# Performance work log

Hardware: AMD Instinct MI355X
Metric: run time of the kernel (lower is better)

## Reference

```python
import jax, jax.numpy as jnp
import numpy as np

N = 1024
D_X = 128
D_Y = 128
NUM_STEPS = 200


def setup_inputs() -> dict:
    key = jax.random.key(0)
    k1, k2, k3, k4, k5 = jax.random.split(key, 5)
    init_samples_x = jax.random.normal(k1, (N, D_X), dtype=jnp.float32)
    init_samples_y = jax.random.normal(k2, (N, D_Y), dtype=jnp.float32)
    mean_final = jax.random.normal(k3, (D_X,), dtype=jnp.float32)
    # variance must be positive and bounded away from zero
    var_final = jax.random.uniform(k4, (D_X,), dtype=jnp.float32, minval=0.25, maxval=0.75)
    gammas = jnp.linspace(1e-3, 1e-2, NUM_STEPS, dtype=jnp.float32)
    # pre-generated per-step Gaussian noise (replaces torch.randn inside the loop)
    noise = jax.random.normal(k5, (NUM_STEPS, N, D_X), dtype=jnp.float32)
    return {
        "init_samples_x": init_samples_x,
        "init_samples_y": init_samples_y,
        "mean_final": mean_final,
        "var_final": var_final,
        "gammas": gammas,
        "noise": noise,
    }


def reference(init_samples_x, init_samples_y, mean_final, var_final, gammas, noise):
    """Faithful JAX port of Langevin.record_init_langevin.

    grad_gauss(x, m, v) = -(x - m) / v
    per step k:
        t_old = x + gamma_k * grad_gauss(x)
        x     = t_old + sqrt(2*gamma_k) * z_k
        t_new = x + gamma_k * grad_gauss(x)
        record x, y, t_old - t_new
    """
    num_steps = gammas.shape[0]
    n = init_samples_x.shape[0]

    def step(x, inp):
        gamma, z = inp
        t_old = x + gamma * (-(x - mean_final) / var_final)
        x_new = t_old + jnp.sqrt(2.0 * gamma) * z
        t_new = x_new + gamma * (-(x_new - mean_final) / var_final)
        return x_new, (x_new, t_old - t_new)

    _, (xs, outs) = jax.lax.scan(step, init_samples_x, (gammas, noise))
    # scan stacks along leading (step) axis -> [S, N, D]; match torch layout [N, S, D]
    x_tot = jnp.transpose(xs, (1, 0, 2))
    out = jnp.transpose(outs, (1, 0, 2))
    # y is constant across steps; the torch loop just replicates it
    y_tot = jnp.broadcast_to(init_samples_y[:, None, :], (n, num_steps, init_samples_y.shape[1]))
    steps_expanded = jnp.broadcast_to(
        jnp.arange(num_steps, dtype=jnp.int32)[None, :, None], (n, num_steps, 1)
    )
    return x_tot, y_tot, out, steps_expanded
```

## Files before the change

### kernel.cpp

```cpp
#include <hip/hip_runtime.h>
#include <math.h>

constexpr int N   = 1024;
constexpr int D   = 128;
constexpr int S   = 200;
constexpr int D2  = D / 2;
constexpr int ND2 = N * D2;
constexpr int CHAIN_BLOCKS = (N * D2) / 256;
constexpr int SEG = 8;
constexpr int L   = S / SEG;
constexpr int PF1 = 10;
constexpr int PF2 = 5;
constexpr int PF  = 8;

typedef float f2 __attribute__((ext_vector_type(2)));
typedef float f4 __attribute__((ext_vector_type(4)));

__global__ __launch_bounds__(256, 4) void boundary_kernel(
    const f2* __restrict__ x0,
    const f2* __restrict__ mean,
    const f2* __restrict__ var,
    const float* __restrict__ gammas,
    const f2* __restrict__ noise,
    f2* __restrict__ bnd)
{
    __shared__ float sg[S];
    __shared__ float ss[S];
    for (int i = threadIdx.x; i < S; i += 256) {
        float g = gammas[i];
        sg[i] = g;
        ss[i] = sqrtf(2.0f * g);
    }
    __syncthreads();

    const int idx = blockIdx.x * 256 + threadIdx.x;
    const int dp  = idx & 63;

    f2 x        = x0[idx];
    const f2 m  = mean[dp];
    const f2 v  = var[dp];
    const float ivx = 1.0f / v.x;
    const float ivy = 1.0f / v.y;

    const f2* zp = noise + idx;

    f2 zb[PF1];
    #pragma unroll
    for (int i = 0; i < PF1; ++i) zb[i] = zp[(size_t)i * ND2];

    #pragma unroll 1
    for (int kb = 0; kb < S; kb += PF1) {
        f2 zn[PF1];
        if (kb + PF1 < S) {
            #pragma unroll
            for (int i = 0; i < PF1; ++i)
                zn[i] = zp[(size_t)(kb + PF1 + i) * ND2];
        }
        #pragma unroll
        for (int i = 0; i < PF1; ++i) {
            const int k = kb + i;
            const float g = sg[k];
            const float s = ss[k];
            const float gx = g * ivx;
            const float gy = g * ivy;
            x.x = fmaf(s, zb[i].x, fmaf(-gx, x.x - m.x, x.x));
            x.y = fmaf(s, zb[i].y, fmaf(-gy, x.y - m.y, x.y));
            if (((k + 1) % L) == 0 && (k + 1) < S)
                bnd[(size_t)((k + 1) / L - 1) * ND2 + idx] = x;
        }
        #pragma unroll
        for (int i = 0; i < PF1; ++i) zb[i] = zn[i];
    }
}

__global__ __launch_bounds__(256, 6) void segment_kernel(
    const f2* __restrict__ x0,
    const f4* __restrict__ y0,
    const f2* __restrict__ mean,
    const f2* __restrict__ var,
    const float* __restrict__ gammas,
    const f2* __restrict__ noise,
    const f2* __restrict__ bnd,
    f2* __restrict__ x_tot,
    f4* __restrict__ y_tot,
    f2* __restrict__ outp,
    float* __restrict__ steps)
{
    if (blockIdx.x >= SEG * CHAIN_BLOCKS) {
        const int n   = blockIdx.x - SEG * CHAIN_BLOCKS;
        const int t   = threadIdx.x;
        const int col = t & 31;
        const int r0  = t >> 5;
        const f4  yv  = y0[(size_t)n * 32 + col];
        f4* yq = y_tot + (size_t)n * (S * 32);
        #pragma unroll
        for (int j = 0; j < S / 8; ++j) {
            const int k = r0 + j * 8;
            __builtin_nontemporal_store(yv, &yq[(size_t)k * 32 + col]);
        }
        if (t < S) steps[(size_t)n * S + t] = (float)t;
        return;
    }

    __shared__ float sg[L];
    __shared__ float ss[L];
    const int seg = blockIdx.x / CHAIN_BLOCKS;
    const int rb  = blockIdx.x % CHAIN_BLOCKS;
    const int k0  = seg * L;
    if (threadIdx.x < L) {
        float g = gammas[k0 + threadIdx.x];
        sg[threadIdx.x] = g;
        ss[threadIdx.x] = sqrtf(2.0f * g);
    }
    __syncthreads();

    const int idx = rb * 256 + threadIdx.x;
    const int n   = idx >> 6;
    const int dp  = idx & 63;

    f2 x = (seg == 0) ? x0[idx] : bnd[(size_t)(seg - 1) * ND2 + idx];
    const f2 m  = mean[dp];
    const f2 v  = var[dp];
    const float ivx = 1.0f / v.x;
    const float ivy = 1.0f / v.y;

    const f2* zp = noise + (size_t)k0 * ND2 + idx;
    f2* xq = x_tot + (size_t)n * (S * D2) + (size_t)k0 * D2 + dp;
    f2* oq = outp  + (size_t)n * (S * D2) + (size_t)k0 * D2 + dp;

    f2 zb[PF2];
    #pragma unroll
    for (int i = 0; i < PF2; ++i) zb[i] = zp[(size_t)i * ND2];

    #pragma unroll 1
    for (int kb = 0; kb < L; kb += PF2) {
        f2 zn[PF2];
        if (kb + PF2 < L) {
            #pragma unroll
            for (int i = 0; i < PF2; ++i)
                zn[i] = zp[(size_t)(kb + PF2 + i) * ND2];
        }
        #pragma unroll
        for (int i = 0; i < PF2; ++i) {
            const int k = kb + i;
            const float g = sg[k];
            const float s = ss[k];
            const float gx = g * ivx;
            const float gy = g * ivy;

            const float tox = fmaf(-gx, x.x - m.x, x.x);
            const float toy = fmaf(-gy, x.y - m.y, x.y);
            x.x = fmaf(s, zb[i].x, tox);
            x.y = fmaf(s, zb[i].y, toy);
            const float tnx = fmaf(-gx, x.x - m.x, x.x);
            const float tny = fmaf(-gy, x.y - m.y, x.y);

            f2 o;
            o.x = tox - tnx;
            o.y = toy - tny;

            __builtin_nontemporal_store(x, &xq[(size_t)k * D2]);
            __builtin_nontemporal_store(o, &oq[(size_t)k * D2]);
        }
        #pragma unroll
        for (int i = 0; i < PF2; ++i) zb[i] = zn[i];
    }
}

__global__ __launch_bounds__(256, 4) void langevin_kernel(
    const f2* __restrict__ x0,
    const f4* __restrict__ y0,
    const f2* __restrict__ mean,
    const f2* __restrict__ var,
    const float* __restrict__ gammas,
    const f2* __restrict__ noise,
    f2* __restrict__ x_tot,
    f4* __restrict__ y_tot,
    f2* __restrict__ outp,
    float* __restrict__ steps)
{
    if (blockIdx.x >= CHAIN_BLOCKS) {
        const int n   = blockIdx.x - CHAIN_BLOCKS;
        const int t   = threadIdx.x;
        const int col = t & 31;
        const int r0  = t >> 5;
        const f4  yv  = y0[(size_t)n * 32 + col];
        f4* yq = y_tot + (size_t)n * (S * 32);
        #pragma unroll
        for (int j = 0; j < S / 8; ++j) {
            const int k = r0 + j * 8;
            __builtin_nontemporal_store(yv, &yq[(size_t)k * 32 + col]);
        }
        if (t < S) steps[(size_t)n * S + t] = (float)t;
        return;
    }

    __shared__ float sg[S];
    __shared__ float ss[S];
    for (int i = threadIdx.x; i < S; i += 256) {
        float g = gammas[i];
        sg[i] = g;
        ss[i] = sqrtf(2.0f * g);
    }
    __syncthreads();

    const int idx = blockIdx.x * 256 + threadIdx.x;
    const int n   = idx >> 6;
    const int dp  = idx & 63;

    f2 x        = x0[idx];
    const f2 m  = mean[dp];
    const f2 v  = var[dp];
    const float ivx = 1.0f / v.x;
    const float ivy = 1.0f / v.y;

    const f2* zp = noise + idx;
    f2* xq = x_tot + (size_t)n * (S * D2) + dp;
    f2* oq = outp  + (size_t)n * (S * D2) + dp;

    f2 zb[PF];
    #pragma unroll
    for (int i = 0; i < PF; ++i)
        zb[i] = __builtin_nontemporal_load(&zp[(size_t)i * ND2]);

    #pragma unroll 1
    for (int kb = 0; kb < S; kb += PF) {
        f2 zn[PF];
        if (kb + PF < S) {
            #pragma unroll
            for (int i = 0; i < PF; ++i)
                zn[i] = __builtin_nontemporal_load(&zp[(size_t)(kb + PF + i) * ND2]);
        }
        #pragma unroll
        for (int i = 0; i < PF; ++i) {
            const int k = kb + i;
            const float g = sg[k];
            const float s = ss[k];
            const float gx = g * ivx;
            const float gy = g * ivy;

            const float tox = fmaf(-gx, x.x - m.x, x.x);
            const float toy = fmaf(-gy, x.y - m.y, x.y);
            x.x = fmaf(s, zb[i].x, tox);
            x.y = fmaf(s, zb[i].y, toy);
            const float tnx = fmaf(-gx, x.x - m.x, x.x);
            const float tny = fmaf(-gy, x.y - m.y, x.y);

            f2 o;
            o.x = tox - tnx;
            o.y = toy - tny;

            __builtin_nontemporal_store(x, &xq[(size_t)k * D2]);
            __builtin_nontemporal_store(o, &oq[(size_t)k * D2]);
        }
        #pragma unroll
        for (int i = 0; i < PF; ++i) zb[i] = zn[i];
    }
}

extern "C" void kernel_launch(void* const* d_in, const int* in_sizes, int n_in,
                              void* d_out, int out_size, void* d_ws, size_t ws_size,
                              hipStream_t stream)
{
    const float* x0     = (const float*)d_in[0];
    const float* y0     = (const float*)d_in[1];
    const float* mean   = (const float*)d_in[2];
    const float* var    = (const float*)d_in[3];
    const float* gammas = (const float*)d_in[4];
    const float* noise  = (const float*)d_in[5];

    float* x_tot = (float*)d_out;
    float* y_tot = x_tot + (size_t)N * S * D;
    float* outp  = y_tot + (size_t)N * S * D;
    float* steps = outp  + (size_t)N * S * D;

    const size_t need = (size_t)(SEG - 1) * ND2 * sizeof(f2);
    if (d_ws != nullptr && ws_size >= need) {
        boundary_kernel<<<CHAIN_BLOCKS, 256, 0, stream>>>(
            (const f2*)x0, (const f2*)mean, (const f2*)var, gammas,
            (const f2*)noise, (f2*)d_ws);
        segment_kernel<<<SEG * CHAIN_BLOCKS + N, 256, 0, stream>>>(
            (const f2*)x0, (const f4*)y0, (const f2*)mean, (const f2*)var,
            gammas, (const f2*)noise, (const f2*)d_ws,
            (f2*)x_tot, (f4*)y_tot, (f2*)outp, steps);
    } else {
        langevin_kernel<<<CHAIN_BLOCKS + N, 256, 0, stream>>>(
            (const f2*)x0, (const f4*)y0, (const f2*)mean, (const f2*)var,
            gammas, (const f2*)noise,
            (f2*)x_tot, (f4*)y_tot, (f2*)outp, steps);
    }
}
```

Measured before the change: 399.6 us.

## Replace sequential boundary pass with parallel linear-recurrence prefix via partial sums

The serial boundary kernel, which walked all 200 steps per element to get segment start values, is replaced by a closed-form solution of the affine recurrence. A tiny single-block kernel precomputes cumulative products and offsets in double precision. A segment-parallel kernel computes weighted noise partial sums per segment, and the emit kernel combines the earlier partials to get each segment's starting x. This removes the long serial dependency chain but adds an extra full read of the noise, double-precision arithmetic, and possible numerical drift from the 1/P scaling.

Result: slower. 460.6 us (+15.3%).

```diff
diff --git a/kernel.cpp b/kernel.cpp
--- a/kernel.cpp
+++ b/kernel.cpp
@@ -9,78 +9,101 @@
 constexpr int CHAIN_BLOCKS = (N * D2) / 256;
 constexpr int SEG = 8;
 constexpr int L   = S / SEG;
-constexpr int PF1 = 10;
 constexpr int PF2 = 5;
 constexpr int PF  = 8;
 
-typedef float f2 __attribute__((ext_vector_type(2)));
-typedef float f4 __attribute__((ext_vector_type(4)));
-
-__global__ __launch_bounds__(256, 4) void boundary_kernel(
-    const f2* __restrict__ x0,
+typedef float  f2 __attribute__((ext_vector_type(2)));
+typedef float  f4 __attribute__((ext_vector_type(4)));
+typedef double d2 __attribute__((ext_vector_type(2)));
+
+constexpr size_t PT_OFF   = 0;
+constexpr size_t QT_OFF   = (size_t)S * D2;
+constexpr size_t CT_OFF   = (size_t)2 * S * D2;
+constexpr size_t PART_OFF = (size_t)3 * S * D2;
+constexpr size_t WS_D2    = PART_OFF + (size_t)SEG * ND2;
+
+__global__ __launch_bounds__(64, 1) void precompute_kernel(
+    const f2* __restrict__ var,
     const f2* __restrict__ mean,
-    const f2* __restrict__ var,
     const float* __restrict__ gammas,
+    d2* __restrict__ ws)
+{
+    const int dp = threadIdx.x;
+    d2* PT = ws + PT_OFF;
+    d2* QT = ws + QT_OFF;
+    d2* CT = ws + CT_OFF;
+
+    const f2 vv = var[dp];
+    const f2 mm = mean[dp];
+    const double vx = vv.x, vy = vv.y, mx = mm.x, my = mm.y;
+    double Px = 1.0, Py = 1.0, Qx = 0.0, Qy = 0.0;
+
+    for (int j = 0; j < S; ++j) {
+        const double g  = (double)gammas[j];
+        Px *= (1.0 - g / vx);
+        Py *= (1.0 - g / vy);
+        const double rx = 1.0 / Px, ry = 1.0 / Py;
+        const double s  = sqrt(2.0 * g);
+        d2 ct; ct.x = s * rx;           ct.y = s * ry;           CT[(size_t)j * D2 + dp] = ct;
+        Qx += (g / vx) * mx * rx;
+        Qy += (g / vy) * my * ry;
+        d2 pt; pt.x = Px; pt.y = Py;    PT[(size_t)j * D2 + dp] = pt;
+        d2 qt; qt.x = Qx; qt.y = Qy;    QT[(size_t)j * D2 + dp] = qt;
+    }
+}
+
+__global__ __launch_bounds__(256, 4) void partial_kernel(
     const f2* __restrict__ noise,
-    f2* __restrict__ bnd)
-{
-    __shared__ float sg[S];
-    __shared__ float ss[S];
-    for (int i = threadIdx.x; i < S; i += 256) {
-        float g = gammas[i];
-        sg[i] = g;
-        ss[i] = sqrtf(2.0f * g);
-    }
-    __syncthreads();
-
-    const int idx = blockIdx.x * 256 + threadIdx.x;
+    d2* __restrict__ ws)
+{
+    const int seg = blockIdx.x / CHAIN_BLOCKS;
+    const int rb  = blockIdx.x % CHAIN_BLOCKS;
+    const int k0  = seg * L;
+    const int idx = rb * 256 + threadIdx.x;
     const int dp  = idx & 63;
 
-    f2 x        = x0[idx];
-    const f2 m  = mean[dp];
-    const f2 v  = var[dp];
-    const float ivx = 1.0f / v.x;
-    const float ivy = 1.0f / v.y;
-
-    const f2* zp = noise + idx;
-
-    f2 zb[PF1];
+    const d2* CT = ws + CT_OFF;
+    const f2* zp = noise + (size_t)k0 * ND2 + idx;
+    const d2* ct = CT + (size_t)k0 * D2 + dp;
+
+    d2 sig; sig.x = 0.0; sig.y = 0.0;
+
+    f2 zb[PF2]; d2 cb[PF2];
     #pragma unroll
-    for (int i = 0; i < PF1; ++i) zb[i] = zp[(size_t)i * ND2];
+    for (int i = 0; i < PF2; ++i) {
+        zb[i] = zp[(size_t)i * ND2];
+        cb[i] = ct[(size_t)i * D2];
+    }
 
     #pragma unroll 1
-    for (int kb = 0; kb < S; kb += PF1) {
-        f2 zn[PF1];
-        if (kb + PF1 < S) {
-            #pragma unroll
-            for (int i = 0; i < PF1; ++i)
-                zn[i] = zp[(size_t)(kb + PF1 + i) * ND2];
-        }
-        #pragma unroll
-        for (int i = 0; i < PF1; ++i) {
-            const int k = kb + i;
-            const float g = sg[k];
-            const float s = ss[k];
-            const float gx = g * ivx;
-            const float gy = g * ivy;
-            x.x = fmaf(s, zb[i].x, fmaf(-gx, x.x - m.x, x.x));
-            x.y = fmaf(s, zb[i].y, fmaf(-gy, x.y - m.y, x.y));
-            if (((k + 1) % L) == 0 && (k + 1) < S)
-                bnd[(size_t)((k + 1) / L - 1) * ND2 + idx] = x;
-        }
-        #pragma unroll
-        for (int i = 0; i < PF1; ++i) zb[i] = zn[i];
-    }
-}
-
-__global__ __launch_bounds__(256, 6) void segment_kernel(
+    for (int kb = 0; kb < L; kb += PF2) {
+        f2 zn[PF2]; d2 cn[PF2];
+        const bool more = (kb + PF2) < L;
+        #pragma unroll
+        for (int i = 0; i < PF2; ++i) {
+            zn[i] = more ? zp[(size_t)(kb + PF2 + i) * ND2] : zb[i];
+            cn[i] = more ? ct[(size_t)(kb + PF2 + i) * D2]  : cb[i];
+        }
+        #pragma unroll
+        for (int i = 0; i < PF2; ++i) {
+            sig.x = fma(cb[i].x, (double)zb[i].x, sig.x);
+            sig.y = fma(cb[i].y, (double)zb[i].y, sig.y);
+        }
+        #pragma unroll
+        for (int i = 0; i < PF2; ++i) { zb[i] = zn[i]; cb[i] = cn[i]; }
+    }
+
+    ws[PART_OFF + (size_t)seg * ND2 + idx] = sig;
+}
+
+__global__ __launch_bounds__(256, 4) void emit_kernel(
     const f2* __restrict__ x0,
     const f4* __restrict__ y0,
     const f2* __restrict__ mean,
     const f2* __restrict__ var,
     const float* __restrict__ gammas,
     const f2* __restrict__ noise,
-    const f2* __restrict__ bnd,
+    const d2* __restrict__ ws,
     f2* __restrict__ x_tot,
     f4* __restrict__ y_tot,
     f2* __restrict__ outp,
@@ -118,33 +141,48 @@
     const int n   = idx >> 6;
     const int dp  = idx & 63;
 
-    f2 x = (seg == 0) ? x0[idx] : bnd[(size_t)(seg - 1) * ND2 + idx];
     const f2 m  = mean[dp];
     const f2 v  = var[dp];
     const float ivx = 1.0f / v.x;
     const float ivy = 1.0f / v.y;
 
-    const f2* zp = noise + (size_t)k0 * ND2 + idx;
+    f2 x;
+    if (seg == 0) {
+        x = x0[idx];
+    } else {
+        d2 W; W.x = 0.0; W.y = 0.0;
+        #pragma unroll 1
+        for (int s2 = 0; s2 < seg; ++s2) {
+            const d2 p = ws[PART_OFF + (size_t)s2 * ND2 + idx];
+            W.x += p.x; W.y += p.y;
+        }
+        const d2 P = ws[PT_OFF + (size_t)(k0 - 1) * D2 + dp];
+        const d2 Q = ws[QT_OFF + (size_t)(k0 - 1) * D2 + dp];
+        const f2 xi = x0[idx];
+        x.x = (float)(P.x * ((double)xi.x + Q.x + W.x));
+        x.y = (float)(P.y * ((double)xi.y + Q.y + W.y));
+    }
+
+    const f2* zq = noise + (size_t)k0 * ND2 + idx;
     f2* xq = x_tot + (size_t)n * (S * D2) + (size_t)k0 * D2 + dp;
     f2* oq = outp  + (size_t)n * (S * D2) + (size_t)k0 * D2 + dp;
 
     f2 zb[PF2];
     #pragma unroll
-    for (int i = 0; i < PF2; ++i) zb[i] = zp[(size_t)i * ND2];
+    for (int i = 0; i < PF2; ++i) zb[i] = zq[(size_t)i * ND2];
 
     #pragma unroll 1
     for (int kb = 0; kb < L; kb += PF2) {
         f2 zn[PF2];
-        if (kb + PF2 < L) {
-            #pragma unroll
-            for (int i = 0; i < PF2; ++i)
-                zn[i] = zp[(size_t)(kb + PF2 + i) * ND2];
-        }
+        const bool more = (k0 + kb + PF2) < S;
+        #pragma unroll
+        for (int i = 0; i < PF2; ++i)
+            zn[i] = more ? zq[(size_t)(kb + PF2 + i) * ND2] : zb[i];
         #pragma unroll
         for (int i = 0; i < PF2; ++i) {
-            const int k = kb + i;
-            const float g = sg[k];
-            const float s = ss[k];
+            const int kk = kb + i;
+            const float g = sg[kk];
+            const float s = ss[kk];
             const float gx = g * ivx;
             const float gy = g * ivy;
 
@@ -159,8 +197,8 @@
             o.x = tox - tnx;
             o.y = toy - tny;
 
-            __builtin_nontemporal_store(x, &xq[(size_t)k * D2]);
-            __builtin_nontemporal_store(o, &oq[(size_t)k * D2]);
+            __builtin_nontemporal_store(x, &xq[(size_t)kk * D2]);
+            __builtin_nontemporal_store(o, &oq[(size_t)kk * D2]);
         }
         #pragma unroll
         for (int i = 0; i < PF2; ++i) zb[i] = zn[i];
@@ -274,14 +312,16 @@
     float* outp  = y_tot + (size_t)N * S * D;
     float* steps = outp  + (size_t)N * S * D;
 
-    const size_t need = (size_t)(SEG - 1) * ND2 * sizeof(f2);
+    const size_t need = WS_D2 * sizeof(d2);
     if (d_ws != nullptr && ws_size >= need) {
-        boundary_kernel<<<CHAIN_BLOCKS, 256, 0, stream>>>(
-            (const f2*)x0, (const f2*)mean, (const f2*)var, gammas,
-            (const f2*)noise, (f2*)d_ws);
-        segment_kernel<<<SEG * CHAIN_BLOCKS + N, 256, 0, stream>>>(
+        d2* ws = (d2*)d_ws;
+        precompute_kernel<<<1, 64, 0, stream>>>(
+            (const f2*)var, (const f2*)mean, gammas, ws);
+        partial_kernel<<<SEG * CHAIN_BLOCKS, 256, 0, stream>>>(
+            (const f2*)noise, ws);
+        emit_kernel<<<SEG * CHAIN_BLOCKS + N, 256, 0, stream>>>(
             (const f2*)x0, (const f4*)y0, (const f2*)mean, (const f2*)var,
-            gammas, (const f2*)noise, (const f2*)d_ws,
+            gammas, (const f2*)noise, ws,
             (f2*)x_tot, (f4*)y_tot, (f2*)outp, steps);
     } else {
         langevin_kernel<<<CHAIN_BLOCKS + N, 256, 0, stream>>>(
```
